# Kernel optimization log

Measured on AMD Instinct MI355X. Metric: run time of the kernel, lower is better.

The kernel has to match this reference:

```python
import jax, jax.numpy as jnp
import numpy as np

T = 32.0                       # softmax temperature
THRESH = float(np.cos(np.pi * 40.0 / 180.0))  # cos(degree), degree=40
NEG_INF = -9.0e15


def setup_inputs() -> dict:
    key = jax.random.key(0)
    ks = jax.random.split(key, 11)
    B, C, D_IMG, D_ATT, H_ATT, H = 2048, 1000, 2048, 312, 128, 128
    def rn(k, shape, scale=1.0):
        return jax.random.normal(k, shape, dtype=jnp.float32) * scale
    return {
        "image_feats": rn(ks[0], (B, D_IMG)),
        "img_proto":   rn(ks[1], (C, D_IMG)),
        "attributes":  rn(ks[2], (C, D_ATT)),
        "unused":      0,
        # parameters
        "att_g":   rn(ks[3], (D_ATT, H_ATT), 0.05),
        "slim_w":  rn(ks[4], (D_IMG, D_ATT), 0.02),   # proto_slim weight (transposed torch layout)
        "slim_b":  rn(ks[5], (D_ATT,), 0.02),
        "img_w":   rn(ks[6], (D_IMG, H), 0.02),
        "proto_w": rn(ks[7], (2 * D_ATT, H), 0.02),   # att_dim + proto_red_dim = 624
        "proto_b": rn(ks[8], (1, H), 0.02),
        "fc_w":    rn(ks[9], (H, 1), 0.05),
        "fc_b":    rn(ks[10], (1,), 0.05),
    }


def reference(image_feats, img_proto, attributes, unused,
              att_g, slim_w, slim_b, img_w, proto_w, proto_b, fc_w, fc_b):
    # proto_slim: [C, D_img] -> [C, att_dim]
    proto_red = img_proto @ slim_w + slim_b

    # --- get_attention: cosine similarity among attribute projections ---
    g = attributes @ att_g                                   # [C, att_hC] (g == h in original)
    gn = g / jnp.clip(jnp.linalg.norm(g, axis=1, keepdims=True), 1e-12)
    sim = gn @ gn.T                                          # [C, C] cosine similarity
    raw = jnp.where(sim > THRESH, sim, NEG_INF)              # threshold mask
    attn = jax.nn.softmax(raw * T, axis=1)                   # [C, C]

    # --- propagate prototypes ---
    att_outs = attn @ attributes                             # [C, att_dim]
    img_proto_outs = attn @ proto_red                        # [C, att_dim]
    outs = jnp.concatenate([att_outs, img_proto_outs], axis=1)  # [C, 2*att_dim]

    # --- relation MLP (broadcast instead of materialized expand+matmul) ---
    img_h = image_feats @ img_w                              # [B, H]
    proto_h = outs @ proto_w                                 # [C, H]
    hidden = jax.nn.relu(img_h[:, None, :] + proto_h[None, :, :] + proto_b)  # [B, C, H]
    outputs = hidden @ fc_w + fc_b                           # [B, C, 1]
    return outputs[..., 0]                                   # [B, C]
```

## Files before the change

kernel.cpp:

```cpp
#include <hip/hip_runtime.h>

typedef unsigned short ushort_t;
typedef __bf16 bf16x8 __attribute__((ext_vector_type(8)));
typedef float f32x4 __attribute__((ext_vector_type(4)));
typedef float f32x2 __attribute__((ext_vector_type(2)));
typedef ushort_t us4 __attribute__((ext_vector_type(4)));

#define T_SOFT 32.0f
#define THRESH 0.76604444311897803f
#define SW 1048
#define SA 72

__device__ __forceinline__ ushort_t f2bf(float f) {
  union { float f; unsigned u; } x; x.f = f;
  unsigned r = (x.u + 0x7fffu + ((x.u >> 16) & 1u)) >> 16;
  return (ushort_t)r;
}
__device__ __forceinline__ float bf2f(ushort_t h) {
  union { unsigned u; float f; } x; x.u = ((unsigned)h) << 16; return x.f;
}

__device__ __forceinline__ us4 pack4(float4 x) {
  union { unsigned u[2]; us4 h; } r;
  union { float4 f; unsigned u[4]; } a;
  a.f = x;
  r.u[0] = __builtin_amdgcn_perm(a.u[1] + 0x8000u, a.u[0] + 0x8000u, 0x07060302u);
  r.u[1] = __builtin_amdgcn_perm(a.u[3] + 0x8000u, a.u[2] + 0x8000u, 0x07060302u);
  return r.h;
}

__device__ __forceinline__ void stage_T(const float* __restrict__ src, int srs, int rbase, int rlimit,
                                        int nbase, ushort_t* __restrict__ dst, int tid) {
  int kg = (tid >> 4) * 4;
  int ns = (tid & 15) * 8;
  float v[4][8];
  #pragma unroll
  for (int i = 0; i < 4; ++i) {
    int r = rbase + kg + i;
    float4 a = make_float4(0.f,0.f,0.f,0.f), c = make_float4(0.f,0.f,0.f,0.f);
    if (r < rlimit) {
      a = *reinterpret_cast<const float4*>(src + (size_t)r * srs + nbase + ns);
      c = *reinterpret_cast<const float4*>(src + (size_t)r * srs + nbase + ns + 4);
    }
    v[i][0]=a.x; v[i][1]=a.y; v[i][2]=a.z; v[i][3]=a.w;
    v[i][4]=c.x; v[i][5]=c.y; v[i][6]=c.z; v[i][7]=c.w;
  }
  #pragma unroll
  for (int j = 0; j < 8; ++j) {
    us4 o;
    o[0] = f2bf(v[0][j]); o[1] = f2bf(v[1][j]); o[2] = f2bf(v[2][j]); o[3] = f2bf(v[3][j]);
    *reinterpret_cast<us4*>(dst + (size_t)(ns + j) * SA + kg) = o;
  }
}

__device__ __forceinline__ void stage_R(const float* __restrict__ src, int srs, int rowbase, int rowmax,
                                        int kbase, int climit, ushort_t* __restrict__ dst, int tid) {
  int frow = tid >> 4;
  int fk = (tid & 15) * 4;
  #pragma unroll
  for (int p = 0; p < 8; ++p) {
    int row = rowbase + frow + p * 16; if (row > rowmax) row = rowmax;
    int k = kbase + fk;
    float4 val = make_float4(0.f,0.f,0.f,0.f);
    if (k < climit) val = *reinterpret_cast<const float4*>(src + (size_t)row * srs + k);
    *reinterpret_cast<us4*>(dst + (size_t)(frow + p * 16) * SA + fk) = pack4(val);
  }
}

__device__ __forceinline__ void stage_Abf(const ushort_t* __restrict__ src, int srs, int kbase,
                                          ushort_t* __restrict__ dst, int tid) {
  int hrow = tid >> 3;
  int hk = (tid & 7) * 8;
  #pragma unroll
  for (int p = 0; p < 4; ++p)
    *reinterpret_cast<bf16x8*>(dst + (size_t)(hrow + p * 32) * SA + hk) =
      *reinterpret_cast<const bf16x8*>(src + (size_t)(hrow + p * 32) * srs + kbase + hk);
}

__device__ __forceinline__ void mfma8(ushort_t* __restrict__ As, ushort_t* __restrict__ Bs,
                                      int tid, f32x4 acc[2][8]) {
  int lane = tid & 63, wv = tid >> 6;
  int l15 = lane & 15, quad = lane >> 4;
  #pragma unroll
  for (int kh = 0; kh < 2; ++kh) {
    bf16x8 af[2];
    #pragma unroll
    for (int pi = 0; pi < 2; ++pi)
      af[pi] = *reinterpret_cast<bf16x8*>(As + ((wv * 2 + pi) * 16 + l15) * SA + kh * 32 + quad * 8);
    #pragma unroll
    for (int ct = 0; ct < 8; ++ct) {
      bf16x8 bfr = *reinterpret_cast<bf16x8*>(Bs + (ct * 16 + l15) * SA + kh * 32 + quad * 8);
      acc[0][ct] = __builtin_amdgcn_mfma_f32_16x16x32_bf16(af[0], bfr, acc[0][ct], 0, 0, 0);
      acc[1][ct] = __builtin_amdgcn_mfma_f32_16x16x32_bf16(af[1], bfr, acc[1][ct], 0, 0, 0);
    }
  }
}

__global__ __launch_bounds__(256) void prep_k(
    const float* __restrict__ attributes, const float* __restrict__ att_g,
    ushort_t* __restrict__ gn_bf,
    const float* __restrict__ image_feats, const float* __restrict__ img_w,
    float* __restrict__ ihp,
    const float* __restrict__ proto_w, const float* __restrict__ slim_w,
    ushort_t* __restrict__ M2T, float* __restrict__ GT_part,
    const float* __restrict__ slim_b, const float* __restrict__ proto_b,
    float* __restrict__ biasG) {
  __shared__ ushort_t As[128 * SA];
  __shared__ ushort_t Bs[128 * SA];
  int b = blockIdx.x, tid = threadIdx.x;
  if (b < 125) {
    __shared__ float a_lds[8][316];
    __shared__ float red2[8][2];
    int h = tid & 127;
    int c0 = b * 8;
    for (int idx = tid; idx < 8 * 312; idx += 256) {
      int r = idx / 312;
      int k = idx - r * 312;
      a_lds[r][k] = attributes[(c0 + r) * 312 + k];
    }
    __syncthreads();
    float acc[8] = {0.f,0.f,0.f,0.f,0.f,0.f,0.f,0.f};
    #pragma unroll 2
    for (int k = 0; k < 312; k += 4) {
      float w0 = att_g[(k + 0) * 128 + h];
      float w1 = att_g[(k + 1) * 128 + h];
      float w2 = att_g[(k + 2) * 128 + h];
      float w3 = att_g[(k + 3) * 128 + h];
      #pragma unroll
      for (int r = 0; r < 8; ++r) {
        float4 a4 = *reinterpret_cast<const float4*>(&a_lds[r][k]);
        acc[r] += a4.x * w0 + a4.y * w1 + a4.z * w2 + a4.w * w3;
      }
    }
    int lane = tid & 63, wvid = (tid >> 6) & 1;
    #pragma unroll
    for (int r = 0; r < 8; ++r) {
      float v = acc[r] * acc[r];
      #pragma unroll
      for (int off = 32; off > 0; off >>= 1) v += __shfl_xor(v, off, 64);
      if (lane == 0) red2[r][wvid] = v;
    }
    __syncthreads();
    #pragma unroll
    for (int r = 0; r < 8; ++r) {
      float nrm = fmaxf(sqrtf(red2[r][0] + red2[r][1]), 1e-12f);
      gn_bf[(c0 + r) * 128 + h] = f2bf(acc[r] / nrm);
    }
    return;
  }
  if (b == 125) {
    us4 z = {0, 0, 0, 0};
    *reinterpret_cast<us4*>(gn_bf + 1000 * 128 + tid * 4) = z;
    return;
  }
  if (b == 126) {
    int h = tid & 127;
    float acc = proto_b[h];
    for (int n = 0; n < 312; n += 4) {
      acc += slim_b[n + 0] * proto_w[(size_t)(312 + n) * 128 + h];
      acc += slim_b[n + 1] * proto_w[(size_t)(313 + n) * 128 + h];
      acc += slim_b[n + 2] * proto_w[(size_t)(314 + n) * 128 + h];
      acc += slim_b[n + 3] * proto_w[(size_t)(315 + n) * 128 + h];
    }
    if (tid < 128) biasG[h] = acc;
    return;
  }
  int lane = tid & 63, wv = tid >> 6;
  int l15 = lane & 15, quad = lane >> 4;
  f32x4 acc[2][8];
  #pragma unroll
  for (int i = 0; i < 2; ++i)
    #pragma unroll
    for (int j = 0; j < 8; ++j) acc[i][j] = f32x4{0.f, 0.f, 0.f, 0.f};

  if (b < 255) {
    int q = b - 127;
    int tile = q >> 3, kc = q & 7;
    int r0 = tile * 128, k0 = kc * 256;
    for (int s = 0; s < 4; ++s) {
      if (s) __syncthreads();
      stage_R(image_feats, 2048, r0, 2047, k0 + s * 64, 1 << 30, As, tid);
      stage_T(img_w, 128, k0 + s * 64, 2048, 0, Bs, tid);
      __syncthreads();
      mfma8(As, Bs, tid, acc);
    }
    float* Cp = ihp + (size_t)kc * 2048 * 128;
    #pragma unroll
    for (int pi = 0; pi < 2; ++pi)
      #pragma unroll
      for (int ct = 0; ct < 8; ++ct) {
        int col = ct * 16 + l15;
        #pragma unroll
        for (int r = 0; r < 4; ++r) {
          int row = r0 + (wv * 2 + pi) * 16 + quad * 4 + r;
          Cp[(size_t)row * 128 + col] = acc[pi][ct][r];
        }
      }
    return;
  }
  if (b < 271) {
    int c0 = (b - 255) * 128;
    for (int s = 0; s < 5; ++s) {
      if (s) __syncthreads();
      stage_T(proto_w, 128, 312 + s * 64, 624, 0, As, tid);
      stage_R(slim_w, 312, c0, 2047, s * 64, 312, Bs, tid);
      __syncthreads();
      mfma8(As, Bs, tid, acc);
    }
    #pragma unroll
    for (int pi = 0; pi < 2; ++pi)
      #pragma unroll
      for (int ct = 0; ct < 8; ++ct) {
        int col = c0 + ct * 16 + l15;
        #pragma unroll
        for (int r = 0; r < 4; ++r) {
          int row = (wv * 2 + pi) * 16 + quad * 4 + r;
          M2T[(size_t)row * 2048 + col] = f2bf(acc[pi][ct][r]);
        }
      }
    return;
  }
  {
    int j0 = (b - 271) * 128;
    for (int s = 0; s < 5; ++s) {
      if (s) __syncthreads();
      stage_T(proto_w, 128, s * 64, 312, 0, As, tid);
      stage_R(attributes, 312, j0, 999, s * 64, 312, Bs, tid);
      __syncthreads();
      mfma8(As, Bs, tid, acc);
    }
    #pragma unroll
    for (int pi = 0; pi < 2; ++pi)
      #pragma unroll
      for (int ct = 0; ct < 8; ++ct) {
        int col = j0 + ct * 16 + l15;
        #pragma unroll
        for (int r = 0; r < 4; ++r) {
          int row = (wv * 2 + pi) * 16 + quad * 4 + r;
          GT_part[(size_t)row * 1024 + col] = acc[pi][ct][r];
        }
      }
  }
}

__global__ __launch_bounds__(256) void red_k(
    const float* __restrict__ ihp, float* __restrict__ img_h,
    const ushort_t* __restrict__ M2T, const float* __restrict__ img_proto,
    float* __restrict__ GT_part) {
  __shared__ ushort_t As[128 * SA];
  __shared__ ushort_t Bs[128 * SA];
  int b = blockIdx.x, tid = threadIdx.x;
  if (b < 128) {
    int t = b * 256 + tid;
    size_t base = (size_t)t * 8;
    #pragma unroll
    for (int g = 0; g < 2; ++g) {
      float4 s = *reinterpret_cast<const float4*>(ihp + base + g * 4);
      #pragma unroll
      for (int c = 1; c < 8; ++c) {
        float4 v = *reinterpret_cast<const float4*>(ihp + (size_t)c * 262144 + base + g * 4);
        s.x += v.x; s.y += v.y; s.z += v.z; s.w += v.w;
      }
      *reinterpret_cast<float4*>(img_h + base + g * 4) = s;
    }
    return;
  }
  int q = b - 128;
  int jt = q >> 2, ch = q & 3;
  int j0 = jt * 128, k0 = ch * 512;
  f32x4 acc[2][8];
  #pragma unroll
  for (int i = 0; i < 2; ++i)
    #pragma unroll
    for (int j = 0; j < 8; ++j) acc[i][j] = f32x4{0.f, 0.f, 0.f, 0.f};
  for (int s = 0; s < 8; ++s) {
    if (s) __syncthreads();
    stage_Abf(M2T, 2048, k0 + s * 64, As, tid);
    stage_R(img_proto, 2048, j0, 999, k0 + s * 64, 1 << 30, Bs, tid);
    __syncthreads();
    mfma8(As, Bs, tid, acc);
  }
  int lane = tid & 63, wv = tid >> 6;
  int l15 = lane & 15, quad = lane >> 4;
  float* dst = GT_part + (size_t)(ch + 1) * 131072;
  #pragma unroll
  for (int pi = 0; pi < 2; ++pi)
    #pragma unroll
    for (int ct = 0; ct < 8; ++ct) {
      int col = j0 + ct * 16 + l15;
      #pragma unroll
      for (int r = 0; r < 4; ++r) {
        int row = (wv * 2 + pi) * 16 + quad * 4 + r;
        dst[(size_t)row * 1024 + col] = acc[pi][ct][r];
      }
    }
}

__global__ __launch_bounds__(256) void gtred_k(const float* __restrict__ GT_part,
                                               const float* __restrict__ biasG,
                                               ushort_t* __restrict__ GT) {
  int t = blockIdx.x * 256 + threadIdx.x;
  size_t base = (size_t)t * 16;
  int row = (int)(base >> 10);
  float bg = biasG[row];
  #pragma unroll
  for (int g = 0; g < 4; ++g) {
    float4 s = *reinterpret_cast<const float4*>(GT_part + base + g * 4);
    #pragma unroll
    for (int c = 1; c < 5; ++c) {
      float4 v = *reinterpret_cast<const float4*>(GT_part + (size_t)c * 131072 + base + g * 4);
      s.x += v.x; s.y += v.y; s.z += v.z; s.w += v.w;
    }
    s.x += bg; s.y += bg; s.z += bg; s.w += bg;
    *reinterpret_cast<us4*>(GT + base + g * 4) = pack4(s);
  }
}

__global__ __launch_bounds__(512) void attn6_k(
    const ushort_t* __restrict__ gn_bf, const ushort_t* __restrict__ GT,
    float* __restrict__ ph) {
  __shared__ ushort_t W[16 * SW];
  __shared__ float rsum[16];
  __shared__ int flags[63];
  int tid = threadIdx.x;
  int i0 = blockIdx.x * 16;
  int lane = tid & 63, wv = tid >> 6;
  int l15 = lane & 15, quad = lane >> 4;
  if (tid < 63) flags[tid] = 0;
  if (tid >= 64 && tid < 80) rsum[tid - 64] = 0.f;
  if (tid < 256) W[(tid >> 4) * SW + 1008 + (tid & 15)] = 0;
  __syncthreads();

  const ushort_t* abase = gn_bf + (size_t)(i0 + l15) * 128 + quad * 8;
  bf16x8 af0 = *reinterpret_cast<const bf16x8*>(abase);
  bf16x8 af1 = *reinterpret_cast<const bf16x8*>(abase + 32);
  bf16x8 af2 = *reinterpret_cast<const bf16x8*>(abase + 64);
  bf16x8 af3 = *reinterpret_cast<const bf16x8*>(abase + 96);
  float rs[4] = {0.f, 0.f, 0.f, 0.f};
  for (int jt = wv; jt < 63; jt += 8) {
    const ushort_t* bbase = gn_bf + (size_t)(jt * 16 + l15) * 128 + quad * 8;
    f32x4 d = {0.f, 0.f, 0.f, 0.f};
    d = __builtin_amdgcn_mfma_f32_16x16x32_bf16(af0, *reinterpret_cast<const bf16x8*>(bbase),      d, 0, 0, 0);
    d = __builtin_amdgcn_mfma_f32_16x16x32_bf16(af1, *reinterpret_cast<const bf16x8*>(bbase + 32), d, 0, 0, 0);
    d = __builtin_amdgcn_mfma_f32_16x16x32_bf16(af2, *reinterpret_cast<const bf16x8*>(bbase + 64), d, 0, 0, 0);
    d = __builtin_amdgcn_mfma_f32_16x16x32_bf16(af3, *reinterpret_cast<const bf16x8*>(bbase + 96), d, 0, 0, 0);
    int hot = 0;
    #pragma unroll
    for (int r = 0; r < 4; ++r) {
      float w = 0.f;
      if (d[r] > THRESH) { w = __expf(T_SOFT * (d[r] - 1.0f)); hot = 1; }
      ushort_t wb = f2bf(w);
      W[(quad * 4 + r) * SW + jt * 16 + l15] = wb;
      rs[r] += bf2f(wb);
    }
    if (hot) flags[jt] = 1;
  }
  #pragma unroll
  for (int r = 0; r < 4; ++r) {
    float v = rs[r];
    v += __shfl_xor(v, 1, 64); v += __shfl_xor(v, 2, 64);
    v += __shfl_xor(v, 4, 64); v += __shfl_xor(v, 8, 64);
    if (l15 == 0) atomicAdd(&rsum[quad * 4 + r], v);
  }
  __syncthreads();

  f32x4 acc2 = {0.f, 0.f, 0.f, 0.f};
  int h = wv * 16 + l15;
  for (int s = 0; s < 32; ++s) {
    int f = flags[2 * s] | ((2 * s + 1 < 63) ? flags[2 * s + 1] : 0);
    if (!f) continue;
    bf16x8 a = *reinterpret_cast<bf16x8*>(W + l15 * SW + s * 32 + quad * 8);
    bf16x8 bfr = *reinterpret_cast<const bf16x8*>(GT + (size_t)h * 1024 + s * 32 + quad * 8);
    acc2 = __builtin_amdgcn_mfma_f32_16x16x32_bf16(a, bfr, acc2, 0, 0, 0);
  }
  #pragma unroll
  for (int r = 0; r < 4; ++r) {
    int row = quad * 4 + r;
    int gi = i0 + row;
    float inv = 1.f / fmaxf(rsum[row], 1e-30f);
    if (gi < 1000) ph[(size_t)gi * 128 + h] = acc2[r] * inv;
  }
}

__global__ __launch_bounds__(256) void final_k(
    const float* __restrict__ img_h, const float* __restrict__ ph,
    const float* __restrict__ fc_w, const float* __restrict__ fc_b,
    float* __restrict__ out) {
  __shared__ float ih[64][132];
  __shared__ float ps[64][132];
  __shared__ float ws_[128];
  int tid = threadIdx.x;
  int b0 = blockIdx.x * 64;
  int c0 = blockIdx.y * 64;
  for (int idx = tid; idx < 2048; idx += 256) {
    int row = idx >> 5, c4 = (idx & 31) * 4;
    float4 v = *reinterpret_cast<const float4*>(img_h + (size_t)(b0 + row) * 128 + c4);
    *reinterpret_cast<float4*>(&ih[row][c4]) = v;
  }
  for (int idx = tid; idx < 2048; idx += 256) {
    int row = idx >> 5, c4 = (idx & 31) * 4;
    int c = c0 + row;
    float4 v = make_float4(0.f, 0.f, 0.f, 0.f);
    if (c < 1000) v = *reinterpret_cast<const float4*>(ph + (size_t)c * 128 + c4);
    *reinterpret_cast<float4*>(&ps[row][c4]) = v;
  }
  if (tid < 128) ws_[tid] = fc_w[tid];
  __syncthreads();
  int tx = tid & 15, ty = tid >> 4;
  f32x2 acc[4][4] = {};
  const f32x2 zero2 = {0.f, 0.f};
  for (int h = 0; h < 128; h += 4) {
    float4 w4 = *reinterpret_cast<float4*>(&ws_[h]);
    f32x2 wlo = {w4.x, w4.y}, whi = {w4.z, w4.w};
    float4 a4[4], p4[4];
    #pragma unroll
    for (int i = 0; i < 4; ++i) a4[i] = *reinterpret_cast<float4*>(&ih[ty * 4 + i][h]);
    #pragma unroll
    for (int j = 0; j < 4; ++j) p4[j] = *reinterpret_cast<float4*>(&ps[tx * 4 + j][h]);
    #pragma unroll
    for (int i = 0; i < 4; ++i) {
      f32x2 alo = {a4[i].x, a4[i].y}, ahi = {a4[i].z, a4[i].w};
      #pragma unroll
      for (int j = 0; j < 4; ++j) {
        f32x2 plo = {p4[j].x, p4[j].y}, phi = {p4[j].z, p4[j].w};
        f32x2 t0 = __builtin_elementwise_max(alo + plo, zero2);
        f32x2 t1 = __builtin_elementwise_max(ahi + phi, zero2);
        acc[i][j] = acc[i][j] + t0 * wlo;
        acc[i][j] = acc[i][j] + t1 * whi;
      }
    }
  }
  float fb = fc_b[0];
  #pragma unroll
  for (int i = 0; i < 4; ++i) {
    int b = b0 + ty * 4 + i;
    int c = c0 + tx * 4;
    if (c < 1000) {
      float4 v = make_float4(acc[i][0].x + acc[i][0].y + fb, acc[i][1].x + acc[i][1].y + fb,
                             acc[i][2].x + acc[i][2].y + fb, acc[i][3].x + acc[i][3].y + fb);
      *reinterpret_cast<float4*>(out + (size_t)b * 1000 + c) = v;
    }
  }
}

extern "C" void kernel_launch(void* const* d_in, const int* in_sizes, int n_in,
                              void* d_out, int out_size, void* d_ws, size_t ws_size,
                              hipStream_t stream) {
  const float* image_feats = (const float*)d_in[0];
  const float* img_proto   = (const float*)d_in[1];
  const float* attributes  = (const float*)d_in[2];
  const float* att_g   = (const float*)d_in[4];
  const float* slim_w  = (const float*)d_in[5];
  const float* slim_b  = (const float*)d_in[6];
  const float* img_w   = (const float*)d_in[7];
  const float* proto_w = (const float*)d_in[8];
  const float* proto_b = (const float*)d_in[9];
  const float* fc_w    = (const float*)d_in[10];
  const float* fc_b    = (const float*)d_in[11];
  float* out = (float*)d_out;

  char* ws = (char*)d_ws;
  size_t o = 0;
  auto alloc = [&](size_t bytes) { size_t r = o; o += (bytes + 255) & ~(size_t)255; return r; };
  ushort_t* gn_bf   = (ushort_t*)(ws + alloc(1008ull * 128 * 2));
  ushort_t* M2T     = (ushort_t*)(ws + alloc(128ull * 2048 * 2));
  ushort_t* GT      = (ushort_t*)(ws + alloc(128ull * 1024 * 2));
  float* biasG     = (float*)(ws + alloc(128ull * 4));
  float* ihp       = (float*)(ws + alloc(8ull * 2048 * 128 * 4));
  float* GT_part   = (float*)(ws + alloc(5ull * 128 * 1024 * 4));
  float* img_h     = (float*)(ws + alloc(2048ull * 128 * 4));
  float* ph        = (float*)(ws + alloc(1000ull * 128 * 4));

  prep_k<<<279, 256, 0, stream>>>(attributes, att_g, gn_bf,
                                  image_feats, img_w, ihp,
                                  proto_w, slim_w, M2T, GT_part,
                                  slim_b, proto_b, biasG);

  red_k<<<160, 256, 0, stream>>>(ihp, img_h, M2T, img_proto, GT_part);

  gtred_k<<<32, 256, 0, stream>>>(GT_part, biasG, GT);

  attn6_k<<<63, 512, 0, stream>>>(gn_bf, GT, ph);

  final_k<<<dim3(32, 16), 256, 0, stream>>>(img_h, ph, fc_w, fc_b, out);
}
```

Measured before the change: 169.0 us.

## Fuse GT reduction into mid kernel, merge attention with final MLP, prefetch staging

Five launches become three. The GT partial reduction moves into the last-arriving block per column tile, chosen with an atomic counter. The attention kernel is fused with the final relation MLP, so ph stays in shared memory, but the attention work is now recomputed for each of 8 batch slices. The img_h GEMM split-K doubles to 16 chunks for more parallelism, and register prefetch of the next tile overlaps global loads with MFMA. The cost is redundant softmax/attention compute and a larger partial-sum reduction.

```diff
diff --git a/kernel.cpp b/kernel.cpp
--- a/kernel.cpp
+++ b/kernel.cpp
@@ -3,7 +3,6 @@
 typedef unsigned short ushort_t;
 typedef __bf16 bf16x8 __attribute__((ext_vector_type(8)));
 typedef float f32x4 __attribute__((ext_vector_type(4)));
-typedef float f32x2 __attribute__((ext_vector_type(2)));
 typedef ushort_t us4 __attribute__((ext_vector_type(4)));
 
 #define T_SOFT 32.0f
@@ -29,11 +28,33 @@
   return r.h;
 }
 
-__device__ __forceinline__ void stage_T(const float* __restrict__ src, int srs, int rbase, int rlimit,
-                                        int nbase, ushort_t* __restrict__ dst, int tid) {
-  int kg = (tid >> 4) * 4;
-  int ns = (tid & 15) * 8;
-  float v[4][8];
+struct RL { float4 v[8]; };
+__device__ __forceinline__ RL r_load(const float* __restrict__ src, int srs, int rowbase, int rowmax,
+                                     int kbase, int climit, int tid) {
+  RL o;
+  int frow = tid >> 4, fk = (tid & 15) * 4;
+  #pragma unroll
+  for (int p = 0; p < 8; ++p) {
+    int row = rowbase + frow + p * 16; if (row > rowmax) row = rowmax;
+    int k = kbase + fk;
+    float4 val = make_float4(0.f, 0.f, 0.f, 0.f);
+    if (k < climit) val = *reinterpret_cast<const float4*>(src + (size_t)row * srs + k);
+    o.v[p] = val;
+  }
+  return o;
+}
+__device__ __forceinline__ void r_store(const RL& o, ushort_t* __restrict__ dst, int tid) {
+  int frow = tid >> 4, fk = (tid & 15) * 4;
+  #pragma unroll
+  for (int p = 0; p < 8; ++p)
+    *reinterpret_cast<us4*>(dst + (size_t)(frow + p * 16) * SA + fk) = pack4(o.v[p]);
+}
+
+struct TL { float v[4][8]; };
+__device__ __forceinline__ TL t_load(const float* __restrict__ src, int srs, int rbase, int rlimit,
+                                     int nbase, int tid) {
+  TL o;
+  int kg = (tid >> 4) * 4, ns = (tid & 15) * 8;
   #pragma unroll
   for (int i = 0; i < 4; ++i) {
     int r = rbase + kg + i;
@@ -42,39 +63,35 @@
       a = *reinterpret_cast<const float4*>(src + (size_t)r * srs + nbase + ns);
       c = *reinterpret_cast<const float4*>(src + (size_t)r * srs + nbase + ns + 4);
     }
-    v[i][0]=a.x; v[i][1]=a.y; v[i][2]=a.z; v[i][3]=a.w;
-    v[i][4]=c.x; v[i][5]=c.y; v[i][6]=c.z; v[i][7]=c.w;
-  }
+    o.v[i][0]=a.x; o.v[i][1]=a.y; o.v[i][2]=a.z; o.v[i][3]=a.w;
+    o.v[i][4]=c.x; o.v[i][5]=c.y; o.v[i][6]=c.z; o.v[i][7]=c.w;
+  }
+  return o;
+}
+__device__ __forceinline__ void t_store(const TL& o, ushort_t* __restrict__ dst, int tid) {
+  int kg = (tid >> 4) * 4, ns = (tid & 15) * 8;
   #pragma unroll
   for (int j = 0; j < 8; ++j) {
-    us4 o;
-    o[0] = f2bf(v[0][j]); o[1] = f2bf(v[1][j]); o[2] = f2bf(v[2][j]); o[3] = f2bf(v[3][j]);
-    *reinterpret_cast<us4*>(dst + (size_t)(ns + j) * SA + kg) = o;
-  }
-}
-
-__device__ __forceinline__ void stage_R(const float* __restrict__ src, int srs, int rowbase, int rowmax,
-                                        int kbase, int climit, ushort_t* __restrict__ dst, int tid) {
-  int frow = tid >> 4;
-  int fk = (tid & 15) * 4;
-  #pragma unroll
-  for (int p = 0; p < 8; ++p) {
-    int row = rowbase + frow + p * 16; if (row > rowmax) row = rowmax;
-    int k = kbase + fk;
-    float4 val = make_float4(0.f,0.f,0.f,0.f);
-    if (k < climit) val = *reinterpret_cast<const float4*>(src + (size_t)row * srs + k);
-    *reinterpret_cast<us4*>(dst + (size_t)(frow + p * 16) * SA + fk) = pack4(val);
-  }
-}
-
-__device__ __forceinline__ void stage_Abf(const ushort_t* __restrict__ src, int srs, int kbase,
-                                          ushort_t* __restrict__ dst, int tid) {
-  int hrow = tid >> 3;
-  int hk = (tid & 7) * 8;
+    us4 w;
+    w[0] = f2bf(o.v[0][j]); w[1] = f2bf(o.v[1][j]); w[2] = f2bf(o.v[2][j]); w[3] = f2bf(o.v[3][j]);
+    *reinterpret_cast<us4*>(dst + (size_t)(ns + j) * SA + kg) = w;
+  }
+}
+
+struct AL { bf16x8 v[4]; };
+__device__ __forceinline__ AL a_load(const ushort_t* __restrict__ src, int srs, int kbase, int tid) {
+  AL o;
+  int hrow = tid >> 3, hk = (tid & 7) * 8;
   #pragma unroll
   for (int p = 0; p < 4; ++p)
-    *reinterpret_cast<bf16x8*>(dst + (size_t)(hrow + p * 32) * SA + hk) =
-      *reinterpret_cast<const bf16x8*>(src + (size_t)(hrow + p * 32) * srs + kbase + hk);
+    o.v[p] = *reinterpret_cast<const bf16x8*>(src + (size_t)(hrow + p * 32) * srs + kbase + hk);
+  return o;
+}
+__device__ __forceinline__ void a_store(const AL& o, ushort_t* __restrict__ dst, int tid) {
+  int hrow = tid >> 3, hk = (tid & 7) * 8;
+  #pragma unroll
+  for (int p = 0; p < 4; ++p)
+    *reinterpret_cast<bf16x8*>(dst + (size_t)(hrow + p * 32) * SA + hk) = o.v[p];
 }
 
 __device__ __forceinline__ void mfma8(ushort_t* __restrict__ As, ushort_t* __restrict__ Bs,
@@ -102,9 +119,9 @@
     const float* __restrict__ image_feats, const float* __restrict__ img_w,
     float* __restrict__ ihp,
     const float* __restrict__ proto_w, const float* __restrict__ slim_w,
-    ushort_t* __restrict__ M2T, float* __restrict__ GT_part,
+    ushort_t* __restrict__ M2T,
     const float* __restrict__ slim_b, const float* __restrict__ proto_b,
-    float* __restrict__ biasG) {
+    float* __restrict__ biasG, int* __restrict__ cnt) {
   __shared__ ushort_t As[128 * SA];
   __shared__ ushort_t Bs[128 * SA];
   int b = blockIdx.x, tid = threadIdx.x;
@@ -151,6 +168,7 @@
   if (b == 125) {
     us4 z = {0, 0, 0, 0};
     *reinterpret_cast<us4*>(gn_bf + 1000 * 128 + tid * 4) = z;
+    if (tid < 8) cnt[tid] = 0;
     return;
   }
   if (b == 126) {
@@ -173,18 +191,25 @@
     #pragma unroll
     for (int j = 0; j < 8; ++j) acc[i][j] = f32x4{0.f, 0.f, 0.f, 0.f};
 
-  if (b < 255) {
+  if (b < 383) {
     int q = b - 127;
-    int tile = q >> 3, kc = q & 7;
-    int r0 = tile * 128, k0 = kc * 256;
-    for (int s = 0; s < 4; ++s) {
+    int tile = q >> 4, kc = q & 15;
+    int r0 = tile * 128, k0 = kc * 128;
+    RL ra = r_load(image_feats, 2048, r0, 2047, k0, 1 << 30, tid);
+    TL tb = t_load(img_w, 128, k0, 2048, 0, tid);
+    #pragma unroll
+    for (int s = 0; s < 2; ++s) {
       if (s) __syncthreads();
-      stage_R(image_feats, 2048, r0, 2047, k0 + s * 64, 1 << 30, As, tid);
-      stage_T(img_w, 128, k0 + s * 64, 2048, 0, Bs, tid);
+      r_store(ra, As, tid);
+      t_store(tb, Bs, tid);
+      if (s == 0) {
+        ra = r_load(image_feats, 2048, r0, 2047, k0 + 64, 1 << 30, tid);
+        tb = t_load(img_w, 128, k0 + 64, 2048, 0, tid);
+      }
       __syncthreads();
       mfma8(As, Bs, tid, acc);
     }
-    float* Cp = ihp + (size_t)kc * 2048 * 128;
+    float* Cp = ihp + (size_t)kc * 262144;
     #pragma unroll
     for (int pi = 0; pi < 2; ++pi)
       #pragma unroll
@@ -198,12 +223,18 @@
       }
     return;
   }
-  if (b < 271) {
-    int c0 = (b - 255) * 128;
+  {
+    int c0 = (b - 383) * 128;
+    TL ta = t_load(proto_w, 128, 312, 624, 0, tid);
+    RL rb = r_load(slim_w, 312, c0, 2047, 0, 312, tid);
     for (int s = 0; s < 5; ++s) {
       if (s) __syncthreads();
-      stage_T(proto_w, 128, 312 + s * 64, 624, 0, As, tid);
-      stage_R(slim_w, 312, c0, 2047, s * 64, 312, Bs, tid);
+      t_store(ta, As, tid);
+      r_store(rb, Bs, tid);
+      if (s + 1 < 5) {
+        ta = t_load(proto_w, 128, 312 + (s + 1) * 64, 624, 0, tid);
+        rb = r_load(slim_w, 312, c0, 2047, (s + 1) * 64, 312, tid);
+      }
       __syncthreads();
       mfma8(As, Bs, tid, acc);
     }
@@ -218,37 +249,18 @@
           M2T[(size_t)row * 2048 + col] = f2bf(acc[pi][ct][r]);
         }
       }
-    return;
-  }
-  {
-    int j0 = (b - 271) * 128;
-    for (int s = 0; s < 5; ++s) {
-      if (s) __syncthreads();
-      stage_T(proto_w, 128, s * 64, 312, 0, As, tid);
-      stage_R(attributes, 312, j0, 999, s * 64, 312, Bs, tid);
-      __syncthreads();
-      mfma8(As, Bs, tid, acc);
-    }
-    #pragma unroll
-    for (int pi = 0; pi < 2; ++pi)
-      #pragma unroll
-      for (int ct = 0; ct < 8; ++ct) {
-        int col = j0 + ct * 16 + l15;
-        #pragma unroll
-        for (int r = 0; r < 4; ++r) {
-          int row = (wv * 2 + pi) * 16 + quad * 4 + r;
-          GT_part[(size_t)row * 1024 + col] = acc[pi][ct][r];
-        }
-      }
-  }
-}
-
-__global__ __launch_bounds__(256) void red_k(
+  }
+}
+
+__global__ __launch_bounds__(256) void mid_k(
     const float* __restrict__ ihp, float* __restrict__ img_h,
     const ushort_t* __restrict__ M2T, const float* __restrict__ img_proto,
-    float* __restrict__ GT_part) {
+    const float* __restrict__ attributes, const float* __restrict__ proto_w,
+    float* __restrict__ GT_part, const float* __restrict__ biasG,
+    ushort_t* __restrict__ GT, int* __restrict__ cnt) {
   __shared__ ushort_t As[128 * SA];
   __shared__ ushort_t Bs[128 * SA];
+  __shared__ int lastv;
   int b = blockIdx.x, tid = threadIdx.x;
   if (b < 128) {
     int t = b * 256 + tid;
@@ -257,7 +269,7 @@
     for (int g = 0; g < 2; ++g) {
       float4 s = *reinterpret_cast<const float4*>(ihp + base + g * 4);
       #pragma unroll
-      for (int c = 1; c < 8; ++c) {
+      for (int c = 1; c < 16; ++c) {
         float4 v = *reinterpret_cast<const float4*>(ihp + (size_t)c * 262144 + base + g * 4);
         s.x += v.x; s.y += v.y; s.z += v.z; s.w += v.w;
       }
@@ -266,23 +278,47 @@
     return;
   }
   int q = b - 128;
-  int jt = q >> 2, ch = q & 3;
-  int j0 = jt * 128, k0 = ch * 512;
-  f32x4 acc[2][8];
-  #pragma unroll
-  for (int i = 0; i < 2; ++i)
-    #pragma unroll
-    for (int j = 0; j < 8; ++j) acc[i][j] = f32x4{0.f, 0.f, 0.f, 0.f};
-  for (int s = 0; s < 8; ++s) {
-    if (s) __syncthreads();
-    stage_Abf(M2T, 2048, k0 + s * 64, As, tid);
-    stage_R(img_proto, 2048, j0, 999, k0 + s * 64, 1 << 30, Bs, tid);
-    __syncthreads();
-    mfma8(As, Bs, tid, acc);
-  }
+  int jt = q / 9, ch = q - jt * 9;
+  int j0 = jt * 128;
   int lane = tid & 63, wv = tid >> 6;
   int l15 = lane & 15, quad = lane >> 4;
-  float* dst = GT_part + (size_t)(ch + 1) * 131072;
+  f32x4 acc[2][8];
+  #pragma unroll
+  for (int i = 0; i < 2; ++i)
+    #pragma unroll
+    for (int j = 0; j < 8; ++j) acc[i][j] = f32x4{0.f, 0.f, 0.f, 0.f};
+  if (ch == 0) {
+    TL ta = t_load(proto_w, 128, 0, 312, 0, tid);
+    RL rb = r_load(attributes, 312, j0, 999, 0, 312, tid);
+    for (int s = 0; s < 5; ++s) {
+      if (s) __syncthreads();
+      t_store(ta, As, tid);
+      r_store(rb, Bs, tid);
+      if (s + 1 < 5) {
+        ta = t_load(proto_w, 128, (s + 1) * 64, 312, 0, tid);
+        rb = r_load(attributes, 312, j0, 999, (s + 1) * 64, 312, tid);
+      }
+      __syncthreads();
+      mfma8(As, Bs, tid, acc);
+    }
+  } else {
+    int k0 = (ch - 1) * 256;
+    AL aa = a_load(M2T, 2048, k0, tid);
+    RL rb = r_load(img_proto, 2048, j0, 999, k0, 1 << 30, tid);
+    #pragma unroll
+    for (int s = 0; s < 4; ++s) {
+      if (s) __syncthreads();
+      a_store(aa, As, tid);
+      r_store(rb, Bs, tid);
+      if (s + 1 < 4) {
+        aa = a_load(M2T, 2048, k0 + (s + 1) * 64, tid);
+        rb = r_load(img_proto, 2048, j0, 999, k0 + (s + 1) * 64, 1 << 30, tid);
+      }
+      __syncthreads();
+      mfma8(As, Bs, tid, acc);
+    }
+  }
+  float* dst = GT_part + (size_t)ch * 131072;
   #pragma unroll
   for (int pi = 0; pi < 2; ++pi)
     #pragma unroll
@@ -294,40 +330,46 @@
         dst[(size_t)row * 1024 + col] = acc[pi][ct][r];
       }
     }
-}
-
-__global__ __launch_bounds__(256) void gtred_k(const float* __restrict__ GT_part,
-                                               const float* __restrict__ biasG,
-                                               ushort_t* __restrict__ GT) {
-  int t = blockIdx.x * 256 + threadIdx.x;
-  size_t base = (size_t)t * 16;
-  int row = (int)(base >> 10);
-  float bg = biasG[row];
-  #pragma unroll
-  for (int g = 0; g < 4; ++g) {
-    float4 s = *reinterpret_cast<const float4*>(GT_part + base + g * 4);
-    #pragma unroll
-    for (int c = 1; c < 5; ++c) {
-      float4 v = *reinterpret_cast<const float4*>(GT_part + (size_t)c * 131072 + base + g * 4);
-      s.x += v.x; s.y += v.y; s.z += v.z; s.w += v.w;
-    }
-    s.x += bg; s.y += bg; s.z += bg; s.w += bg;
-    *reinterpret_cast<us4*>(GT + base + g * 4) = pack4(s);
-  }
-}
-
-__global__ __launch_bounds__(512) void attn6_k(
+  __threadfence();
+  if (tid == 0) lastv = atomicAdd(&cnt[jt], 1);
+  __syncthreads();
+  if (lastv == 8) {
+    __threadfence();
+    int row = tid >> 1;
+    int cb = j0 + (tid & 1) * 64;
+    float bg = biasG[row];
+    #pragma unroll
+    for (int e = 0; e < 16; ++e) {
+      size_t off = (size_t)row * 1024 + cb + e * 4;
+      float4 s = *reinterpret_cast<const float4*>(GT_part + off);
+      #pragma unroll
+      for (int c = 1; c < 9; ++c) {
+        float4 v = *reinterpret_cast<const float4*>(GT_part + (size_t)c * 131072 + off);
+        s.x += v.x; s.y += v.y; s.z += v.z; s.w += v.w;
+      }
+      s.x += bg; s.y += bg; s.z += bg; s.w += bg;
+      *reinterpret_cast<us4*>(GT + off) = pack4(s);
+    }
+  }
+}
+
+__global__ __launch_bounds__(512) void attnfin_k(
     const ushort_t* __restrict__ gn_bf, const ushort_t* __restrict__ GT,
-    float* __restrict__ ph) {
+    const float* __restrict__ img_h, const float* __restrict__ fc_w,
+    const float* __restrict__ fc_b, float* __restrict__ out) {
   __shared__ ushort_t W[16 * SW];
+  __shared__ float ps[16][132];
   __shared__ float rsum[16];
   __shared__ int flags[63];
+  __shared__ float ws_[128];
   int tid = threadIdx.x;
   int i0 = blockIdx.x * 16;
+  int b0c = blockIdx.y * 256;
   int lane = tid & 63, wv = tid >> 6;
   int l15 = lane & 15, quad = lane >> 4;
   if (tid < 63) flags[tid] = 0;
   if (tid >= 64 && tid < 80) rsum[tid - 64] = 0.f;
+  if (tid < 128) ws_[tid] = fc_w[tid];
   if (tid < 256) W[(tid >> 4) * SW + 1008 + (tid & 15)] = 0;
   __syncthreads();
 
@@ -376,70 +418,30 @@
   #pragma unroll
   for (int r = 0; r < 4; ++r) {
     int row = quad * 4 + r;
-    int gi = i0 + row;
     float inv = 1.f / fmaxf(rsum[row], 1e-30f);
-    if (gi < 1000) ph[(size_t)gi * 128 + h] = acc2[r] * inv;
-  }
-}
-
-__global__ __launch_bounds__(256) void final_k(
-    const float* __restrict__ img_h, const float* __restrict__ ph,
-    const float* __restrict__ fc_w, const float* __restrict__ fc_b,
-    float* __restrict__ out) {
-  __shared__ float ih[64][132];
-  __shared__ float ps[64][132];
-  __shared__ float ws_[128];
-  int tid = threadIdx.x;
-  int b0 = blockIdx.x * 64;
-  int c0 = blockIdx.y * 64;
-  for (int idx = tid; idx < 2048; idx += 256) {
-    int row = idx >> 5, c4 = (idx & 31) * 4;
-    float4 v = *reinterpret_cast<const float4*>(img_h + (size_t)(b0 + row) * 128 + c4);
-    *reinterpret_cast<float4*>(&ih[row][c4]) = v;
-  }
-  for (int idx = tid; idx < 2048; idx += 256) {
-    int row = idx >> 5, c4 = (idx & 31) * 4;
-    int c = c0 + row;
-    float4 v = make_float4(0.f, 0.f, 0.f, 0.f);
-    if (c < 1000) v = *reinterpret_cast<const float4*>(ph + (size_t)c * 128 + c4);
-    *reinterpret_cast<float4*>(&ps[row][c4]) = v;
-  }
-  if (tid < 128) ws_[tid] = fc_w[tid];
+    ps[row][h] = acc2[r] * inv;
+  }
   __syncthreads();
+
   int tx = tid & 15, ty = tid >> 4;
-  f32x2 acc[4][4] = {};
-  const f32x2 zero2 = {0.f, 0.f};
-  for (int h = 0; h < 128; h += 4) {
-    float4 w4 = *reinterpret_cast<float4*>(&ws_[h]);
-    f32x2 wlo = {w4.x, w4.y}, whi = {w4.z, w4.w};
-    float4 a4[4], p4[4];
-    #pragma unroll
-    for (int i = 0; i < 4; ++i) a4[i] = *reinterpret_cast<float4*>(&ih[ty * 4 + i][h]);
-    #pragma unroll
-    for (int j = 0; j < 4; ++j) p4[j] = *reinterpret_cast<float4*>(&ps[tx * 4 + j][h]);
-    #pragma unroll
-    for (int i = 0; i < 4; ++i) {
-      f32x2 alo = {a4[i].x, a4[i].y}, ahi = {a4[i].z, a4[i].w};
-      #pragma unroll
-      for (int j = 0; j < 4; ++j) {
-        f32x2 plo = {p4[j].x, p4[j].y}, phi = {p4[j].z, p4[j].w};
-        f32x2 t0 = __builtin_elementwise_max(alo + plo, zero2);
-        f32x2 t1 = __builtin_elementwise_max(ahi + phi, zero2);
-        acc[i][j] = acc[i][j] + t0 * wlo;
-        acc[i][j] = acc[i][j] + t1 * whi;
-      }
-    }
-  }
-  float fb = fc_b[0];
-  #pragma unroll
-  for (int i = 0; i < 4; ++i) {
-    int b = b0 + ty * 4 + i;
-    int c = c0 + tx * 4;
-    if (c < 1000) {
-      float4 v = make_float4(acc[i][0].x + acc[i][0].y + fb, acc[i][1].x + acc[i][1].y + fb,
-                             acc[i][2].x + acc[i][2].y + fb, acc[i][3].x + acc[i][3].y + fb);
-      *reinterpret_cast<float4*>(out + (size_t)b * 1000 + c) = v;
-    }
+  int c = i0 + tx;
+  int bb = b0c + ty * 8;
+  float accf[8] = {0.f,0.f,0.f,0.f,0.f,0.f,0.f,0.f};
+  for (int hh = 0; hh < 128; hh += 4) {
+    float4 w4 = *reinterpret_cast<float4*>(&ws_[hh]);
+    float4 p4 = *reinterpret_cast<float4*>(&ps[tx][hh]);
+    #pragma unroll
+    for (int i = 0; i < 8; ++i) {
+      float4 a4 = *reinterpret_cast<const float4*>(img_h + (size_t)(bb + i) * 128 + hh);
+      accf[i] += fmaxf(a4.x + p4.x, 0.f) * w4.x + fmaxf(a4.y + p4.y, 0.f) * w4.y
+               + fmaxf(a4.z + p4.z, 0.f) * w4.z + fmaxf(a4.w + p4.w, 0.f) * w4.w;
+    }
+  }
+  if (c < 1000) {
+    float fb = fc_b[0];
+    #pragma unroll
+    for (int i = 0; i < 8; ++i)
+      out[(size_t)(bb + i) * 1000 + c] = accf[i] + fb;
   }
 }
 
@@ -466,21 +468,18 @@
   ushort_t* M2T     = (ushort_t*)(ws + alloc(128ull * 2048 * 2));
   ushort_t* GT      = (ushort_t*)(ws + alloc(128ull * 1024 * 2));
   float* biasG     = (float*)(ws + alloc(128ull * 4));
-  float* ihp       = (float*)(ws + alloc(8ull * 2048 * 128 * 4));
-  float* GT_part   = (float*)(ws + alloc(5ull * 128 * 1024 * 4));
+  float* ihp       = (float*)(ws + alloc(16ull * 2048 * 128 * 4));
+  float* GT_part   = (float*)(ws + alloc(9ull * 128 * 1024 * 4));
   float* img_h     = (float*)(ws + alloc(2048ull * 128 * 4));
-  float* ph        = (float*)(ws + alloc(1000ull * 128 * 4));
-
-  prep_k<<<279, 256, 0, stream>>>(attributes, att_g, gn_bf,
+  int*   cnt       = (int*)(ws + alloc(256));
+
+  prep_k<<<399, 256, 0, stream>>>(attributes, att_g, gn_bf,
                                   image_feats, img_w, ihp,
-                                  proto_w, slim_w, M2T, GT_part,
-                                  slim_b, proto_b, biasG);
-
-  red_k<<<160, 256, 0, stream>>>(ihp, img_h, M2T, img_proto, GT_part);
-
-  gtred_k<<<32, 256, 0, stream>>>(GT_part, biasG, GT);
-
-  attn6_k<<<63, 512, 0, stream>>>(gn_bf, GT, ph);
-
-  final_k<<<dim3(32, 16), 256, 0, stream>>>(img_h, ph, fc_w, fc_b, out);
-}
+                                  proto_w, slim_w, M2T,
+                                  slim_b, proto_b, biasG, cnt);
+
+  mid_k<<<200, 256, 0, stream>>>(ihp, img_h, M2T, img_proto,
+                                 attributes, proto_w, GT_part, biasG, GT, cnt);
+
+  attnfin_k<<<dim3(63, 8), 512, 0, stream>>>(gn_bf, GT, img_h, fc_w, fc_b, out);
+}
```

After: 207.6 us. 22.9% more time.
